# Kernel optimization log

Measured on AMD Instinct MI355X. Metric: run time of the kernel, lower is better.

The kernel has to match this reference:

```python
import jax, jax.numpy as jnp
import numpy as np

NUM_VARS = 22
LAYERS = 2
N = 2 ** NUM_VARS


def setup_inputs() -> dict:
    key = jax.random.key(0)
    k1, k2, k3, k4 = jax.random.split(key, 4)
    h = jax.random.normal(k1, (N,), dtype=jnp.float32)          # unsatisfied-clause 'energy' per bitstring
    hS = jax.random.uniform(k2, (N,), dtype=jnp.float32)        # satisfiability weight per bitstring
    gamma = jax.random.normal(k3, (LAYERS,), dtype=jnp.float32) * 0.01
    beta = jax.random.normal(k4, (LAYERS,), dtype=jnp.float32) * 0.01
    return {"h": h, "hS": hS, "gamma": gamma, "beta": beta}


def reference(h, hS, gamma, beta):
    n = NUM_VARS
    # |+>^n initial state: uniform amplitudes 1/sqrt(N)
    circuit = jnp.full((N,), 1.0 / np.sqrt(N), dtype=jnp.complex64)
    for l in range(LAYERS):
        # cost unitary: elementwise phase exp(i * gamma * h)
        circuit = jnp.exp((1j * gamma[l] * h).astype(jnp.complex64)) * circuit
        # mixing unitary: per-qubit X-rotation butterfly.
        # torch's transpose(0,i)+split+cat swaps the two slices along qubit axis i,
        # which for a size-2 axis is exactly a flip along that axis.
        cb = jnp.cos(beta[l]).astype(jnp.complex64)
        sb = (1j * jnp.sin(beta[l])).astype(jnp.complex64)
        c = circuit.reshape((2,) * n)
        for i in range(n):  # fixed small loop over qubits (structurally distinct axes)
            c = cb * c + sb * jnp.flip(c, axis=i)
        circuit = c.reshape(N)
    ps = jnp.real(circuit * jnp.conj(circuit))  # |amplitude|^2
    return jnp.dot(ps, hS)
```

## Files before the change

kernel.cpp:

```cpp
#include <hip/hip_runtime.h>


#define NTOT    (1u << 22)
#define LO_BITS 13
#define HI_BITS 9
#define LO      (1u << LO_BITS)
#define HI      (1u << HI_BITS)
#define GRP     32
#define TPB     512
#define TPB2    1024
#define R       16

typedef __fp16 h2_t __attribute__((ext_vector_type(2)));
union PkU { unsigned u; h2_t h; };

__device__ __forceinline__ unsigned pk(float x, float y) {
    PkU p; p.h = __builtin_amdgcn_cvt_pkrtz(x, y); return p.u;
}
__device__ __forceinline__ float2 unpk(unsigned v) {
    PkU p; p.u = v; return make_float2((float)p.h.x, (float)p.h.y);
}

#define REGSTAGE(MASK, CB, SB) {                                  \
    _Pragma("unroll")                                             \
    for (int r0 = 0; r0 < R; ++r0) {                              \
        if ((r0 & (MASK)) == 0) {                                 \
            const int r1 = r0 | (MASK);                           \
            float t0r = re[r0], t0i = im[r0];                     \
            float t1r = re[r1], t1i = im[r1];                     \
            re[r0] = (CB) * t0r - (SB) * t1i;                     \
            im[r0] = (CB) * t0i + (SB) * t1r;                     \
            re[r1] = (CB) * t1r - (SB) * t0i;                     \
            im[r1] = (CB) * t1i + (SB) * t0r;                     \
        } } }

#define SHFLSTAGE(MASK, CB, SB) {                                 \
    _Pragma("unroll")                                             \
    for (int r = 0; r < R; ++r) {                                 \
        unsigned pv = (unsigned)__shfl_xor((int)pk(re[r], im[r]), (MASK), 64); \
        float2 p = unpk(pv);                                      \
        float tr = re[r], ti = im[r];                             \
        re[r] = (CB) * tr - (SB) * p.y;                           \
        im[r] = (CB) * ti + (SB) * p.x;                           \
    } }

__global__ __launch_bounds__(TPB, 4) void k_init_low(
    const float* __restrict__ h, const float* __restrict__ gam,
    const float* __restrict__ bet, unsigned* __restrict__ st,
    float* __restrict__ out)
{
    __shared__ unsigned sC[LO];
    const float g1 = gam[0];
    const float cb = __cosf(bet[0]), sb = __sinf(bet[0]);
    const unsigned t = threadIdx.x, lane = t & 63u, wave = t >> 6;
    const size_t base = (size_t)blockIdx.x * LO;
    float re[R], im[R];

    if (blockIdx.x == 0 && t == 0) out[0] = 0.f;

    #pragma unroll
    for (int r = 0; r < R; ++r) {
        float s, c;
        __sincosf(g1 * h[base + (unsigned)r * TPB + t], &s, &c);
        re[r] = c * 0x1p-11f;
        im[r] = s * 0x1p-11f;
    }
    REGSTAGE(1, cb, sb)  REGSTAGE(2, cb, sb)
    REGSTAGE(4, cb, sb)  REGSTAGE(8, cb, sb)
    SHFLSTAGE(1,  cb, sb) SHFLSTAGE(2,  cb, sb)
    SHFLSTAGE(4,  cb, sb) SHFLSTAGE(8,  cb, sb)
    SHFLSTAGE(16, cb, sb) SHFLSTAGE(32, cb, sb)
    #pragma unroll
    for (int r = 0; r < R; ++r) sC[(unsigned)r * TPB + t] = pk(re[r], im[r]);
    __syncthreads();
    #pragma unroll
    for (int r = 0; r < R; ++r) {
        unsigned j = lane | ((unsigned)(r & 7) << 6) | (wave << 9) | ((unsigned)(r >> 3) << 12);
        float2 v = unpk(sC[j]); re[r] = v.x; im[r] = v.y;
    }
    REGSTAGE(1, cb, sb)  REGSTAGE(2, cb, sb)  REGSTAGE(4, cb, sb)
    #pragma unroll
    for (int r = 0; r < R; ++r) {
        unsigned j = lane | ((unsigned)(r & 7) << 6) | (wave << 9) | ((unsigned)(r >> 3) << 12);
        st[base + j] = pk(re[r], im[r]);
    }
}

__global__ __launch_bounds__(TPB2, 4) void k_high(
    const float* __restrict__ h, const float* __restrict__ gam,
    const float* __restrict__ bet, unsigned* __restrict__ st)
{
    __shared__ unsigned sC[GRP * HI];
    const float g2  = gam[1];
    const float cb1 = __cosf(bet[0]), sb1 = __sinf(bet[0]);
    const float cb2 = __cosf(bet[1]), sb2 = __sinf(bet[1]);
    const unsigned t = threadIdx.x, lane = t & 63u, w = t >> 6;
    const unsigned g  = lane & 31u;
    const unsigned h0 = lane >> 5;
    const unsigned lo0 = blockIdx.x * GRP;
    float re[R], im[R];

    #pragma unroll
    for (int r = 0; r < R; ++r) {
        unsigned hi = h0 | (w << 1) | ((unsigned)r << 5);
        float2 v = unpk(st[(size_t)hi * LO + lo0 + g]);
        re[r] = v.x; im[r] = v.y;
    }
    REGSTAGE(1, cb1, sb1)  REGSTAGE(2, cb1, sb1)
    REGSTAGE(4, cb1, sb1)  REGSTAGE(8, cb1, sb1)
    SHFLSTAGE(32, cb1, sb1)
    #pragma unroll
    for (int r = 0; r < R; ++r)
        sC[g | (h0 << 5) | (w << 6) | ((unsigned)r << 10)] = pk(re[r], im[r]);
    __syncthreads();
    #pragma unroll
    for (int r = 0; r < R; ++r) {
        float2 v = unpk(sC[g | (h0 << 5) | ((unsigned)r << 6) | (w << 10)]);
        re[r] = v.x; im[r] = v.y;
    }
    REGSTAGE(1, cb1, sb1)  REGSTAGE(2, cb1, sb1)
    REGSTAGE(4, cb1, sb1)  REGSTAGE(8, cb1, sb1)
    #pragma unroll
    for (int r = 0; r < R; ++r) {
        unsigned hi = h0 | ((unsigned)r << 1) | (w << 5);
        float s, c;
        __sincosf(g2 * h[(size_t)hi * LO + lo0 + g], &s, &c);
        float tr = re[r], ti = im[r];
        re[r] = tr * c - ti * s;
        im[r] = tr * s + ti * c;
    }
    REGSTAGE(1, cb2, sb2)  REGSTAGE(2, cb2, sb2)
    REGSTAGE(4, cb2, sb2)  REGSTAGE(8, cb2, sb2)
    SHFLSTAGE(32, cb2, sb2)
    __syncthreads();
    #pragma unroll
    for (int r = 0; r < R; ++r)
        sC[g | (h0 << 5) | ((unsigned)r << 6) | (w << 10)] = pk(re[r], im[r]);
    __syncthreads();
    #pragma unroll
    for (int r = 0; r < R; ++r) {
        float2 v = unpk(sC[g | (h0 << 5) | (w << 6) | ((unsigned)r << 10)]);
        re[r] = v.x; im[r] = v.y;
    }
    REGSTAGE(1, cb2, sb2)  REGSTAGE(2, cb2, sb2)
    REGSTAGE(4, cb2, sb2)  REGSTAGE(8, cb2, sb2)
    #pragma unroll
    for (int r = 0; r < R; ++r) {
        unsigned hi = h0 | (w << 1) | ((unsigned)r << 5);
        st[(size_t)hi * LO + lo0 + g] = pk(re[r], im[r]);
    }
}

__global__ __launch_bounds__(TPB, 4) void k_low2(
    const float* __restrict__ hS, const float* __restrict__ bet,
    const unsigned* __restrict__ st, float* __restrict__ out)
{
    __shared__ unsigned sC[LO];
    __shared__ float wsum[TPB / 64];
    const float cb = __cosf(bet[1]), sb = __sinf(bet[1]);
    const unsigned t = threadIdx.x, lane = t & 63u, wave = t >> 6;
    const size_t base = (size_t)blockIdx.x * LO;
    float re[R], im[R];

    #pragma unroll
    for (int r = 0; r < R; ++r) {
        float2 v = unpk(st[base + (unsigned)r * TPB + t]);
        re[r] = v.x; im[r] = v.y;
    }
    REGSTAGE(1, cb, sb)  REGSTAGE(2, cb, sb)
    REGSTAGE(4, cb, sb)  REGSTAGE(8, cb, sb)
    SHFLSTAGE(1,  cb, sb) SHFLSTAGE(2,  cb, sb)
    SHFLSTAGE(4,  cb, sb) SHFLSTAGE(8,  cb, sb)
    SHFLSTAGE(16, cb, sb) SHFLSTAGE(32, cb, sb)
    #pragma unroll
    for (int r = 0; r < R; ++r) sC[(unsigned)r * TPB + t] = pk(re[r], im[r]);
    __syncthreads();
    #pragma unroll
    for (int r = 0; r < R; ++r) {
        unsigned j = lane | ((unsigned)(r & 7) << 6) | (wave << 9) | ((unsigned)(r >> 3) << 12);
        float2 v = unpk(sC[j]); re[r] = v.x; im[r] = v.y;
    }
    REGSTAGE(1, cb, sb)  REGSTAGE(2, cb, sb)  REGSTAGE(4, cb, sb)
    float acc = 0.f;
    #pragma unroll
    for (int r = 0; r < R; ++r) {
        unsigned j = lane | ((unsigned)(r & 7) << 6) | (wave << 9) | ((unsigned)(r >> 3) << 12);
        acc = fmaf(re[r] * re[r] + im[r] * im[r], hS[base + j], acc);
    }
    #pragma unroll
    for (int off = 32; off >= 1; off >>= 1)
        acc += __shfl_down(acc, off, 64);
    if (lane == 0) wsum[wave] = acc;
    __syncthreads();
    if (t == 0) {
        float s = 0.f;
        #pragma unroll
        for (int w = 0; w < TPB / 64; ++w) s += wsum[w];
        unsafeAtomicAdd(out, s);
    }
}

extern "C" void kernel_launch(void* const* d_in, const int* in_sizes, int n_in,
                              void* d_out, int out_size, void* d_ws, size_t ws_size,
                              hipStream_t stream)
{
    (void)in_sizes; (void)n_in; (void)out_size; (void)ws_size;
    const float* h   = (const float*)d_in[0];
    const float* hS  = (const float*)d_in[1];
    const float* gam = (const float*)d_in[2];
    const float* bet = (const float*)d_in[3];
    unsigned* st = (unsigned*)d_ws;
    float* out   = (float*)d_out;

    k_init_low<<<dim3(NTOT / LO), dim3(TPB),  0, stream>>>(h, gam, bet, st, out);
    k_high    <<<dim3(LO / GRP),  dim3(TPB2), 0, stream>>>(h, gam, bet, st);
    k_low2    <<<dim3(NTOT / LO), dim3(TPB),  0, stream>>>(hS, bet, st, out);
}
```

Measured before the change: 120.6 us.

## Rebalance low/high qubit split to 14/8 bits and prefetch h/hS loads

```diff
diff --git a/kernel.cpp b/kernel.cpp
--- a/kernel.cpp
+++ b/kernel.cpp
@@ -2,13 +2,12 @@
 
 
 #define NTOT    (1u << 22)
-#define LO_BITS 13
-#define HI_BITS 9
+#define LO_BITS 14
+#define HI_BITS 8
 #define LO      (1u << LO_BITS)
 #define HI      (1u << HI_BITS)
-#define GRP     32
-#define TPB     512
-#define TPB2    1024
+#define GRP     64
+#define TPB     1024
 #define R       16
 
 typedef __fp16 h2_t __attribute__((ext_vector_type(2)));
@@ -52,7 +51,7 @@
     __shared__ unsigned sC[LO];
     const float g1 = gam[0];
     const float cb = __cosf(bet[0]), sb = __sinf(bet[0]);
-    const unsigned t = threadIdx.x, lane = t & 63u, wave = t >> 6;
+    const unsigned t = threadIdx.x, lane = t & 63u, w = t >> 6;
     const size_t base = (size_t)blockIdx.x * LO;
     float re[R], im[R];
 
@@ -61,7 +60,7 @@
     #pragma unroll
     for (int r = 0; r < R; ++r) {
         float s, c;
-        __sincosf(g1 * h[base + (unsigned)r * TPB + t], &s, &c);
+        __sincosf(g1 * h[base + ((unsigned)r << 10) + t], &s, &c);
         re[r] = c * 0x1p-11f;
         im[r] = s * 0x1p-11f;
     }
@@ -71,22 +70,23 @@
     SHFLSTAGE(4,  cb, sb) SHFLSTAGE(8,  cb, sb)
     SHFLSTAGE(16, cb, sb) SHFLSTAGE(32, cb, sb)
     #pragma unroll
-    for (int r = 0; r < R; ++r) sC[(unsigned)r * TPB + t] = pk(re[r], im[r]);
-    __syncthreads();
-    #pragma unroll
-    for (int r = 0; r < R; ++r) {
-        unsigned j = lane | ((unsigned)(r & 7) << 6) | (wave << 9) | ((unsigned)(r >> 3) << 12);
+    for (int r = 0; r < R; ++r) sC[((unsigned)r << 10) | t] = pk(re[r], im[r]);
+    __syncthreads();
+    #pragma unroll
+    for (int r = 0; r < R; ++r) {
+        unsigned j = (w << 10) | ((unsigned)r << 6) | lane;
         float2 v = unpk(sC[j]); re[r] = v.x; im[r] = v.y;
     }
-    REGSTAGE(1, cb, sb)  REGSTAGE(2, cb, sb)  REGSTAGE(4, cb, sb)
-    #pragma unroll
-    for (int r = 0; r < R; ++r) {
-        unsigned j = lane | ((unsigned)(r & 7) << 6) | (wave << 9) | ((unsigned)(r >> 3) << 12);
+    REGSTAGE(1, cb, sb)  REGSTAGE(2, cb, sb)
+    REGSTAGE(4, cb, sb)  REGSTAGE(8, cb, sb)
+    #pragma unroll
+    for (int r = 0; r < R; ++r) {
+        unsigned j = (w << 10) | ((unsigned)r << 6) | lane;
         st[base + j] = pk(re[r], im[r]);
     }
 }
 
-__global__ __launch_bounds__(TPB2, 4) void k_high(
+__global__ __launch_bounds__(TPB, 4) void k_high(
     const float* __restrict__ h, const float* __restrict__ gam,
     const float* __restrict__ bet, unsigned* __restrict__ st)
 {
@@ -94,59 +94,59 @@
     const float g2  = gam[1];
     const float cb1 = __cosf(bet[0]), sb1 = __sinf(bet[0]);
     const float cb2 = __cosf(bet[1]), sb2 = __sinf(bet[1]);
-    const unsigned t = threadIdx.x, lane = t & 63u, w = t >> 6;
-    const unsigned g  = lane & 31u;
-    const unsigned h0 = lane >> 5;
+    const unsigned t = threadIdx.x, g = t & 63u, w = t >> 6;
     const unsigned lo0 = blockIdx.x * GRP;
-    float re[R], im[R];
-
-    #pragma unroll
-    for (int r = 0; r < R; ++r) {
-        unsigned hi = h0 | (w << 1) | ((unsigned)r << 5);
+    float re[R], im[R], hv[R];
+
+    #pragma unroll
+    for (int r = 0; r < R; ++r) {
+        unsigned hi = w | ((unsigned)r << 4);
         float2 v = unpk(st[(size_t)hi * LO + lo0 + g]);
         re[r] = v.x; im[r] = v.y;
+    }
+    #pragma unroll
+    for (int r = 0; r < R; ++r) {
+        unsigned hi = (unsigned)r | (w << 4);
+        hv[r] = h[(size_t)hi * LO + lo0 + g];
     }
     REGSTAGE(1, cb1, sb1)  REGSTAGE(2, cb1, sb1)
     REGSTAGE(4, cb1, sb1)  REGSTAGE(8, cb1, sb1)
-    SHFLSTAGE(32, cb1, sb1)
     #pragma unroll
     for (int r = 0; r < R; ++r)
-        sC[g | (h0 << 5) | (w << 6) | ((unsigned)r << 10)] = pk(re[r], im[r]);
-    __syncthreads();
-    #pragma unroll
-    for (int r = 0; r < R; ++r) {
-        float2 v = unpk(sC[g | (h0 << 5) | ((unsigned)r << 6) | (w << 10)]);
+        sC[g | (w << 6) | ((unsigned)r << 10)] = pk(re[r], im[r]);
+    __syncthreads();
+    #pragma unroll
+    for (int r = 0; r < R; ++r) {
+        float2 v = unpk(sC[g | ((unsigned)r << 6) | (w << 10)]);
         re[r] = v.x; im[r] = v.y;
     }
     REGSTAGE(1, cb1, sb1)  REGSTAGE(2, cb1, sb1)
     REGSTAGE(4, cb1, sb1)  REGSTAGE(8, cb1, sb1)
     #pragma unroll
     for (int r = 0; r < R; ++r) {
-        unsigned hi = h0 | ((unsigned)r << 1) | (w << 5);
         float s, c;
-        __sincosf(g2 * h[(size_t)hi * LO + lo0 + g], &s, &c);
+        __sincosf(g2 * hv[r], &s, &c);
         float tr = re[r], ti = im[r];
         re[r] = tr * c - ti * s;
         im[r] = tr * s + ti * c;
     }
     REGSTAGE(1, cb2, sb2)  REGSTAGE(2, cb2, sb2)
     REGSTAGE(4, cb2, sb2)  REGSTAGE(8, cb2, sb2)
-    SHFLSTAGE(32, cb2, sb2)
     __syncthreads();
     #pragma unroll
     for (int r = 0; r < R; ++r)
-        sC[g | (h0 << 5) | ((unsigned)r << 6) | (w << 10)] = pk(re[r], im[r]);
-    __syncthreads();
-    #pragma unroll
-    for (int r = 0; r < R; ++r) {
-        float2 v = unpk(sC[g | (h0 << 5) | (w << 6) | ((unsigned)r << 10)]);
+        sC[g | ((unsigned)r << 6) | (w << 10)] = pk(re[r], im[r]);
+    __syncthreads();
+    #pragma unroll
+    for (int r = 0; r < R; ++r) {
+        float2 v = unpk(sC[g | (w << 6) | ((unsigned)r << 10)]);
         re[r] = v.x; im[r] = v.y;
     }
     REGSTAGE(1, cb2, sb2)  REGSTAGE(2, cb2, sb2)
     REGSTAGE(4, cb2, sb2)  REGSTAGE(8, cb2, sb2)
     #pragma unroll
     for (int r = 0; r < R; ++r) {
-        unsigned hi = h0 | (w << 1) | ((unsigned)r << 5);
+        unsigned hi = w | ((unsigned)r << 4);
         st[(size_t)hi * LO + lo0 + g] = pk(re[r], im[r]);
     }
 }
@@ -156,16 +156,20 @@
     const unsigned* __restrict__ st, float* __restrict__ out)
 {
     __shared__ unsigned sC[LO];
-    __shared__ float wsum[TPB / 64];
     const float cb = __cosf(bet[1]), sb = __sinf(bet[1]);
-    const unsigned t = threadIdx.x, lane = t & 63u, wave = t >> 6;
+    const unsigned t = threadIdx.x, lane = t & 63u, w = t >> 6;
     const size_t base = (size_t)blockIdx.x * LO;
-    float re[R], im[R];
-
-    #pragma unroll
-    for (int r = 0; r < R; ++r) {
-        float2 v = unpk(st[base + (unsigned)r * TPB + t]);
-        re[r] = v.x; im[r] = v.y;
+    float re[R], im[R], hv[R];
+
+    #pragma unroll
+    for (int r = 0; r < R; ++r) {
+        float2 v = unpk(st[base + ((unsigned)r << 10) + t]);
+        re[r] = v.x; im[r] = v.y;
+    }
+    #pragma unroll
+    for (int r = 0; r < R; ++r) {
+        unsigned j = (w << 10) | ((unsigned)r << 6) | lane;
+        hv[r] = hS[base + j];
     }
     REGSTAGE(1, cb, sb)  REGSTAGE(2, cb, sb)
     REGSTAGE(4, cb, sb)  REGSTAGE(8, cb, sb)
@@ -173,29 +177,29 @@
     SHFLSTAGE(4,  cb, sb) SHFLSTAGE(8,  cb, sb)
     SHFLSTAGE(16, cb, sb) SHFLSTAGE(32, cb, sb)
     #pragma unroll
-    for (int r = 0; r < R; ++r) sC[(unsigned)r * TPB + t] = pk(re[r], im[r]);
-    __syncthreads();
-    #pragma unroll
-    for (int r = 0; r < R; ++r) {
-        unsigned j = lane | ((unsigned)(r & 7) << 6) | (wave << 9) | ((unsigned)(r >> 3) << 12);
+    for (int r = 0; r < R; ++r) sC[((unsigned)r << 10) | t] = pk(re[r], im[r]);
+    __syncthreads();
+    #pragma unroll
+    for (int r = 0; r < R; ++r) {
+        unsigned j = (w << 10) | ((unsigned)r << 6) | lane;
         float2 v = unpk(sC[j]); re[r] = v.x; im[r] = v.y;
     }
-    REGSTAGE(1, cb, sb)  REGSTAGE(2, cb, sb)  REGSTAGE(4, cb, sb)
+    REGSTAGE(1, cb, sb)  REGSTAGE(2, cb, sb)
+    REGSTAGE(4, cb, sb)  REGSTAGE(8, cb, sb)
     float acc = 0.f;
     #pragma unroll
-    for (int r = 0; r < R; ++r) {
-        unsigned j = lane | ((unsigned)(r & 7) << 6) | (wave << 9) | ((unsigned)(r >> 3) << 12);
-        acc = fmaf(re[r] * re[r] + im[r] * im[r], hS[base + j], acc);
-    }
+    for (int r = 0; r < R; ++r)
+        acc = fmaf(re[r] * re[r] + im[r] * im[r], hv[r], acc);
     #pragma unroll
     for (int off = 32; off >= 1; off >>= 1)
         acc += __shfl_down(acc, off, 64);
-    if (lane == 0) wsum[wave] = acc;
+    __syncthreads();
+    if (lane == 0) ((float*)sC)[w] = acc;
     __syncthreads();
     if (t == 0) {
         float s = 0.f;
         #pragma unroll
-        for (int w = 0; w < TPB / 64; ++w) s += wsum[w];
+        for (int ww = 0; ww < TPB / 64; ++ww) s += ((float*)sC)[ww];
         unsafeAtomicAdd(out, s);
     }
 }
@@ -212,7 +216,7 @@
     unsigned* st = (unsigned*)d_ws;
     float* out   = (float*)d_out;
 
-    k_init_low<<<dim3(NTOT / LO), dim3(TPB),  0, stream>>>(h, gam, bet, st, out);
-    k_high    <<<dim3(LO / GRP),  dim3(TPB2), 0, stream>>>(h, gam, bet, st);
-    k_low2    <<<dim3(NTOT / LO), dim3(TPB),  0, stream>>>(hS, bet, st, out);
-}
+    k_init_low<<<dim3(NTOT / LO), dim3(TPB), 0, stream>>>(h, gam, bet, st, out);
+    k_high    <<<dim3(LO / GRP),  dim3(TPB), 0, stream>>>(h, gam, bet, st);
+    k_low2    <<<dim3(NTOT / LO), dim3(TPB), 0, stream>>>(hS, bet, st, out);
+}
```

After: 119.4 us. Within noise of the previous version (-1.0%).
